# Optimization experiments

Measured on AMD Instinct MI355X. Metric: run time of the kernel, lower is better.

Reference implementation:

```python
import jax, jax.numpy as jnp
import numpy as np

GROUP_SIZE = 128
IN_FEATURES = 8192
OUT_FEATURES = 28672
TOKENS = 32


def _dequantize(qweight, qzeros, scales):
    """ExLlama q4 dequant.
    qweight: (K//8, N) int32, 8 int4 values per word packed along k.
    qzeros:  (G, N//8) int32, 8 int4 zeros per word packed along n.
    scales:  (G, N) fp16.  g = k // GROUP_SIZE; w = s * (q - (z + 1)).
    """
    shifts = jnp.arange(8, dtype=jnp.int32) * 4
    K = qweight.shape[0] * 8
    N = qweight.shape[1]
    G = qzeros.shape[0]
    # unpack weights along k: (K//8, 8, N) -> (K, N)
    q = (qweight[:, None, :] >> shifts[None, :, None]) & 15
    q = q.reshape(K, N)
    # unpack zeros along n: (G, N//8, 8) -> (G, N)
    z = (qzeros[:, :, None] >> shifts[None, None, :]) & 15
    z = z.reshape(G, N)
    # group-wise dequant: reshape k into (G, GROUP_SIZE)
    qg = q.reshape(G, GROUP_SIZE, N).astype(jnp.float16)
    zf = (z + 1).astype(jnp.float16)[:, None, :]          # ExLlama stores zero-1
    w = (qg - zf) * scales[:, None, :]                    # (G, GS, N) fp16
    return w.reshape(K, N)


def setup_inputs() -> dict:
    key = jax.random.key(0)
    k1, k2, k3, k4, k5 = jax.random.split(key, 5)
    x = jax.random.normal(k1, (TOKENS, IN_FEATURES), dtype=jnp.float16)
    qweight = jax.random.randint(k2, (IN_FEATURES // 8, OUT_FEATURES),
                                 minval=-(2**31), maxval=2**31 - 1, dtype=jnp.int32)
    qzeros = jax.random.randint(k3, (IN_FEATURES // GROUP_SIZE, OUT_FEATURES // 8),
                                minval=-(2**31), maxval=2**31 - 1, dtype=jnp.int32)
    scales = (jax.random.uniform(k4, (IN_FEATURES // GROUP_SIZE, OUT_FEATURES),
                                 dtype=jnp.float32) * 0.01 + 0.001).astype(jnp.float16)
    bias = jax.random.normal(k5, (OUT_FEATURES,), dtype=jnp.float16)
    return {"x": x, "qweight": qweight, "qzeros": qzeros,
            "scales": scales, "bias": bias}


def reference(x, qweight, qzeros, scales, bias):
    w = _dequantize(qweight, qzeros, scales)              # (K, N) fp16
    out = jnp.matmul(x.astype(jnp.float16), w)            # (T, N)
    return out + bias
```

## Files before the change

### kernel.cpp

```cpp
#include <hip/hip_runtime.h>

#define T_TOK   32
#define KDIM    8192
#define NDIM    28672
#define NZW     3584
#define NSEG    16
#define SEGK    (KDIM / NSEG)
#define GPS     (NSEG == 16 ? 4 : 4)
#define XROW    (SEGK + 8)
#define XIT     ((T_TOK * SEGK) / (256 * 8))

typedef _Float16 half8  __attribute__((ext_vector_type(8)));
typedef _Float16 half2v __attribute__((ext_vector_type(2)));
typedef float    f32x4  __attribute__((ext_vector_type(4)));
typedef unsigned uint4v __attribute__((ext_vector_type(4)));

template<bool ATOMIC>
__global__ __launch_bounds__(256)
void exllama_gemm16(const int*   __restrict__ qweight,
                    const int*   __restrict__ qzeros,
                    const float* __restrict__ scales,
                    const float* __restrict__ x,
                    const float* __restrict__ bias,
                    float*       __restrict__ ws,
                    float*       __restrict__ out)
{
    __shared__ alignas(16) _Float16 xs[T_TOK * XROW];

    const int tid  = threadIdx.x;
    const int lane = tid & 63;
    const int wav  = tid >> 6;
    const int quad = lane >> 4;
    const int l16  = lane & 15;
    const int seg  = blockIdx.y;
    const int n0   = blockIdx.x * 256 + wav * 64;
    const int g0   = seg * GPS;

    int nc[4];
    #pragma unroll
    for (int j = 0; j < 4; ++j) nc[j] = n0 + j * 16 + l16;

    auto LOADQW = [&](unsigned* qw, int g) {
        const size_t rb = (size_t)((g0 + g) * 16 + quad) * NDIM;
        #pragma unroll
        for (int c = 0; c < 4; ++c)
            #pragma unroll
            for (int j = 0; j < 4; ++j)
                qw[c * 4 + j] = (unsigned)qweight[rb + (size_t)(c * 4) * NDIM + nc[j]];
    };

    unsigned qwA[16], qwB[16];
    LOADQW(qwA, 0);

    float sraw[GPS][4];
    int   zraw[GPS][4];
    #pragma unroll
    for (int g = 0; g < GPS; ++g)
        #pragma unroll
        for (int j = 0; j < 4; ++j) {
            sraw[g][j] = scales[(size_t)(g0 + g) * NDIM + nc[j]];
            zraw[g][j] = qzeros[(size_t)(g0 + g) * NZW + (nc[j] >> 3)];
        }

    {
        const int kseg0 = seg * SEGK;
        #pragma unroll
        for (int it = 0; it < XIT; ++it) {
            const int e  = it * 2048 + tid * 8;
            const int t  = e >> 9;
            const int kl = e & (SEGK - 1);
            const float* xp = x + (size_t)t * KDIM + kseg0 + kl;
            f32x4 lo = *(const f32x4*)xp;
            f32x4 hi = *(const f32x4*)(xp + 4);
            uint4v u;
            #pragma unroll
            for (int j = 0; j < 4; ++j)
                u[j] = __builtin_bit_cast(unsigned,
                          __builtin_amdgcn_cvt_pkrtz(lo[j], hi[j]));
            *(uint4v*)(xs + t * XROW + kl) = u;
        }
    }

    half2v sp[GPS][4], cp[GPS][4];
    #pragma unroll
    for (int g = 0; g < GPS; ++g)
        #pragma unroll
        for (int j = 0; j < 4; ++j) {
            const int z = (zraw[g][j] >> ((nc[j] & 7) * 4)) & 15;
            const _Float16 sh = (_Float16)sraw[g][j];
            const _Float16 ch = (_Float16)(float)(-(1025 + z));
            sp[g][j] = (half2v){sh, sh};
            cp[g][j] = (half2v){ch, ch};
        }

    __syncthreads();

    f32x4 acc[4][2];
    #pragma unroll
    for (int j = 0; j < 4; ++j)
        #pragma unroll
        for (int m = 0; m < 2; ++m)
            acc[j][m] = (f32x4){0.f, 0.f, 0.f, 0.f};

    auto COMPUTEG = [&](const unsigned* qw, int g) {
        #pragma unroll
        for (int c = 0; c < 4; ++c) {
            const int kloc = g * 128 + c * 32 + quad * 8;
            half8 a0 = *(const half8*)(xs + l16 * XROW + kloc);
            half8 a1 = *(const half8*)(xs + (l16 + 16) * XROW + kloc);
            #pragma unroll
            for (int j = 0; j < 4; ++j) {
                const unsigned w = qw[c * 4 + j];
                uint4v bu;
                #pragma unroll
                for (int i = 0; i < 4; ++i) {
                    unsigned t = ((w >> (4 * i)) & 0x000F000Fu) | 0x64006400u;
                    half2v th = __builtin_bit_cast(half2v, t);
                    half2v r  = (th + cp[g][j]) * sp[g][j];
                    bu[i] = __builtin_bit_cast(unsigned, r);
                }
                half8 bf = __builtin_bit_cast(half8, bu);
                acc[j][0] = __builtin_amdgcn_mfma_f32_16x16x32_f16(a0, bf, acc[j][0], 0, 0, 0);
                acc[j][1] = __builtin_amdgcn_mfma_f32_16x16x32_f16(a1, bf, acc[j][1], 0, 0, 0);
            }
        }
    };

    LOADQW(qwB, 1);
    COMPUTEG(qwA, 0);
    LOADQW(qwA, 2);
    COMPUTEG(qwB, 1);
    LOADQW(qwB, 3);
    COMPUTEG(qwA, 2);
    COMPUTEG(qwB, 3);

    if (ATOMIC) {
        #pragma unroll
        for (int j = 0; j < 4; ++j) {
            const float bb = bias[nc[j]] * (1.0f / NSEG);
            #pragma unroll
            for (int m = 0; m < 2; ++m)
                #pragma unroll
                for (int r = 0; r < 4; ++r) {
                    const int t = m * 16 + quad * 4 + r;
                    unsafeAtomicAdd(out + (size_t)t * NDIM + nc[j], acc[j][m][r] + bb);
                }
        }
    } else {
        float* wsp = ws + (size_t)seg * (T_TOK * NDIM);
        #pragma unroll
        for (int j = 0; j < 4; ++j)
            #pragma unroll
            for (int m = 0; m < 2; ++m)
                #pragma unroll
                for (int r = 0; r < 4; ++r) {
                    const int t = m * 16 + quad * 4 + r;
                    wsp[(size_t)t * NDIM + nc[j]] = acc[j][m][r];
                }
    }
}

__global__ __launch_bounds__(256)
void reduce_bias(const float* __restrict__ ws,
                 const float* __restrict__ bias,
                 float*       __restrict__ out)
{
    const int e = (blockIdx.x * 256 + threadIdx.x) * 4;
    const int n = e % NDIM;
    f32x4 sum = (f32x4){0.f, 0.f, 0.f, 0.f};
    #pragma unroll
    for (int s = 0; s < NSEG; ++s)
        sum += *(const f32x4*)(ws + (size_t)s * (T_TOK * NDIM) + e);
    f32x4 bb = *(const f32x4*)(bias + n);
    *(f32x4*)(out + e) = sum + bb;
}

extern "C" void kernel_launch(void* const* d_in, const int* in_sizes, int n_in,
                              void* d_out, int out_size, void* d_ws, size_t ws_size,
                              hipStream_t stream)
{
    const float* x  = (const float*)d_in[0];
    const int* qweight = (const int*)d_in[1];
    const int* qzeros  = (const int*)d_in[2];
    const float* sc = (const float*)d_in[3];
    const float* bs = (const float*)d_in[4];
    float* out      = (float*)d_out;

    const size_t need = (size_t)NSEG * T_TOK * NDIM * sizeof(float);
    if (ws_size >= need) {
        exllama_gemm16<false><<<dim3(NDIM / 256, NSEG), 256, 0, stream>>>(
            qweight, qzeros, sc, x, bs, (float*)d_ws, out);
        reduce_bias<<<(T_TOK * NDIM) / (256 * 4), 256, 0, stream>>>(
            (const float*)d_ws, bs, out);
    } else {
        exllama_gemm16<true><<<dim3(NDIM / 256, NSEG), 256, 0, stream>>>(
            qweight, qzeros, sc, x, bs, nullptr, out);
    }
}
```

Before: 208.0 us.

## Store split-K partials in fp16, swizzle LDS, pack scale/zero, pin schedule

Split-K partial sums are written to the workspace as fp16 instead of fp32, halving the workspace write and reduce-read traffic. The padded LDS activation tile is replaced by an XOR-swizzled layout, scale and zero are packed into one half2 per column to cut registers, and launch_bounds requests 5 waves per SIMD. The second weight prefetch is hoisted earlier and sched_barriers pin the load/compute order. Rounding 16 partials to fp16 before summing adds precision loss.

```diff
diff --git a/kernel.cpp b/kernel.cpp
--- a/kernel.cpp
+++ b/kernel.cpp
@@ -6,26 +6,27 @@
 #define NZW     3584
 #define NSEG    16
 #define SEGK    (KDIM / NSEG)
-#define GPS     (NSEG == 16 ? 4 : 4)
-#define XROW    (SEGK + 8)
+#define GPS     4
 #define XIT     ((T_TOK * SEGK) / (256 * 8))
 
 typedef _Float16 half8  __attribute__((ext_vector_type(8)));
+typedef _Float16 half4  __attribute__((ext_vector_type(4)));
 typedef _Float16 half2v __attribute__((ext_vector_type(2)));
 typedef float    f32x4  __attribute__((ext_vector_type(4)));
 typedef unsigned uint4v __attribute__((ext_vector_type(4)));
 
 template<bool ATOMIC>
-__global__ __launch_bounds__(256)
+__global__ __launch_bounds__(256, 5)
 void exllama_gemm16(const int*   __restrict__ qweight,
                     const int*   __restrict__ qzeros,
                     const float* __restrict__ scales,
                     const float* __restrict__ x,
                     const float* __restrict__ bias,
-                    float*       __restrict__ ws,
+                    _Float16*    __restrict__ ws,
                     float*       __restrict__ out)
 {
-    __shared__ alignas(16) _Float16 xs[T_TOK * XROW];
+    __shared__ alignas(16) _Float16 xs[T_TOK * SEGK];
+    char* xb = (char*)xs;
 
     const int tid  = threadIdx.x;
     const int lane = tid & 63;
@@ -51,6 +52,7 @@
 
     unsigned qwA[16], qwB[16];
     LOADQW(qwA, 0);
+    LOADQW(qwB, 1);
 
     float sraw[GPS][4];
     int   zraw[GPS][4];
@@ -77,20 +79,19 @@
             for (int j = 0; j < 4; ++j)
                 u[j] = __builtin_bit_cast(unsigned,
                           __builtin_amdgcn_cvt_pkrtz(lo[j], hi[j]));
-            *(uint4v*)(xs + t * XROW + kl) = u;
-        }
-    }
-
-    half2v sp[GPS][4], cp[GPS][4];
+            const int off = (t * 1024 + kl * 2) ^ ((t & 7) << 4);
+            *(uint4v*)(xb + off) = u;
+        }
+    }
+
+    half2v scp[GPS][4];
     #pragma unroll
     for (int g = 0; g < GPS; ++g)
         #pragma unroll
         for (int j = 0; j < 4; ++j) {
             const int z = (zraw[g][j] >> ((nc[j] & 7) * 4)) & 15;
-            const _Float16 sh = (_Float16)sraw[g][j];
-            const _Float16 ch = (_Float16)(float)(-(1025 + z));
-            sp[g][j] = (half2v){sh, sh};
-            cp[g][j] = (half2v){ch, ch};
+            scp[g][j] = (half2v){(_Float16)sraw[g][j],
+                                 (_Float16)(float)(-(1025 + z))};
         }
 
     __syncthreads();
@@ -106,17 +107,21 @@
         #pragma unroll
         for (int c = 0; c < 4; ++c) {
             const int kloc = g * 128 + c * 32 + quad * 8;
-            half8 a0 = *(const half8*)(xs + l16 * XROW + kloc);
-            half8 a1 = *(const half8*)(xs + (l16 + 16) * XROW + kloc);
+            const int o0 = (l16 * 1024 + kloc * 2) ^ ((l16 & 7) << 4);
+            half8 a0 = *(const half8*)(xb + o0);
+            half8 a1 = *(const half8*)(xb + o0 + 16 * 1024);
             #pragma unroll
             for (int j = 0; j < 4; ++j) {
                 const unsigned w = qw[c * 4 + j];
+                const half2v sc = scp[g][j];
+                const half2v s2 = (half2v){sc[0], sc[0]};
+                const half2v c2 = (half2v){sc[1], sc[1]};
                 uint4v bu;
                 #pragma unroll
                 for (int i = 0; i < 4; ++i) {
                     unsigned t = ((w >> (4 * i)) & 0x000F000Fu) | 0x64006400u;
                     half2v th = __builtin_bit_cast(half2v, t);
-                    half2v r  = (th + cp[g][j]) * sp[g][j];
+                    half2v r  = (th + c2) * s2;
                     bu[i] = __builtin_bit_cast(unsigned, r);
                 }
                 half8 bf = __builtin_bit_cast(half8, bu);
@@ -126,11 +131,12 @@
         }
     };
 
-    LOADQW(qwB, 1);
     COMPUTEG(qwA, 0);
     LOADQW(qwA, 2);
+    __builtin_amdgcn_sched_barrier(0);
     COMPUTEG(qwB, 1);
     LOADQW(qwB, 3);
+    __builtin_amdgcn_sched_barrier(0);
     COMPUTEG(qwA, 2);
     COMPUTEG(qwB, 3);
 
@@ -147,7 +153,7 @@
                 }
         }
     } else {
-        float* wsp = ws + (size_t)seg * (T_TOK * NDIM);
+        _Float16* wsp = ws + (size_t)seg * (T_TOK * NDIM);
         #pragma unroll
         for (int j = 0; j < 4; ++j)
             #pragma unroll
@@ -155,22 +161,25 @@
                 #pragma unroll
                 for (int r = 0; r < 4; ++r) {
                     const int t = m * 16 + quad * 4 + r;
-                    wsp[(size_t)t * NDIM + nc[j]] = acc[j][m][r];
+                    wsp[(size_t)t * NDIM + nc[j]] = (_Float16)acc[j][m][r];
                 }
     }
 }
 
 __global__ __launch_bounds__(256)
-void reduce_bias(const float* __restrict__ ws,
-                 const float* __restrict__ bias,
-                 float*       __restrict__ out)
+void reduce_bias(const _Float16* __restrict__ ws,
+                 const float*    __restrict__ bias,
+                 float*          __restrict__ out)
 {
     const int e = (blockIdx.x * 256 + threadIdx.x) * 4;
     const int n = e % NDIM;
     f32x4 sum = (f32x4){0.f, 0.f, 0.f, 0.f};
     #pragma unroll
-    for (int s = 0; s < NSEG; ++s)
-        sum += *(const f32x4*)(ws + (size_t)s * (T_TOK * NDIM) + e);
+    for (int s = 0; s < NSEG; ++s) {
+        half4 v = *(const half4*)(ws + (size_t)s * (T_TOK * NDIM) + e);
+        #pragma unroll
+        for (int i = 0; i < 4; ++i) sum[i] += (float)v[i];
+    }
     f32x4 bb = *(const f32x4*)(bias + n);
     *(f32x4*)(out + e) = sum + bb;
 }
@@ -186,12 +195,12 @@
     const float* bs = (const float*)d_in[4];
     float* out      = (float*)d_out;
 
-    const size_t need = (size_t)NSEG * T_TOK * NDIM * sizeof(float);
+    const size_t need = (size_t)NSEG * T_TOK * NDIM * sizeof(_Float16);
     if (ws_size >= need) {
         exllama_gemm16<false><<<dim3(NDIM / 256, NSEG), 256, 0, stream>>>(
-            qweight, qzeros, sc, x, bs, (float*)d_ws, out);
+            qweight, qzeros, sc, x, bs, (_Float16*)d_ws, out);
         reduce_bias<<<(T_TOK * NDIM) / (256 * 4), 256, 0, stream>>>(
-            (const float*)d_ws, bs, out);
+            (const _Float16*)d_ws, bs, out);
     } else {
         exllama_gemm16<true><<<dim3(NDIM / 256, NSEG), 256, 0, stream>>>(
             qweight, qzeros, sc, x, bs, nullptr, out);
```

Result: slower. 255.4 us (+22.8%).
